# Optimization experiments

Measured on AMD Instinct MI355X. Metric: run time of the kernel, lower is better.

## Reference

```python
import jax, jax.numpy as jnp
import numpy as np

# Quantum circuit closed form: per wire i, state |0> -> RX(x_i) -> RY(theta_i),
# then <PauliZ_i> = cos(theta_i) * cos(x_i). No entangling gates, so wires are
# independent and the whole per-token loop collapses to one elementwise op.

B, S, E = 8, 4096, 512
NQ, FFN = 8, 2048

def setup_inputs() -> dict:
    key = jax.random.key(0)
    ks = jax.random.split(key, 6)
    return {
        "x": jax.random.normal(ks[0], (B, S, E), dtype=jnp.float32),
        "theta": jax.random.normal(ks[1], (NQ,), dtype=jnp.float32),
        "W1": jax.random.normal(ks[2], (FFN, NQ), dtype=jnp.float32) * (1.0 / np.sqrt(NQ)),
        "b1": jax.random.normal(ks[3], (FFN,), dtype=jnp.float32) * 0.01,
        "W2": jax.random.normal(ks[4], (E, FFN), dtype=jnp.float32) * (1.0 / np.sqrt(FFN)),
        "b2": jax.random.normal(ks[5], (E,), dtype=jnp.float32) * 0.01,
    }

def reference(x, theta, W1, b1, W2, b2):
    n_qubits = theta.shape[0]
    # token_slice = x[:, :, :n_qubits]; <Z> = cos(theta) * cos(x)
    q_out = jnp.cos(x[..., :n_qubits]) * jnp.cos(theta)        # [B, S, NQ]
    h = jax.nn.relu(jnp.einsum('bsq,fq->bsf', q_out, W1) + b1)  # [B, S, FFN]
    out = jnp.einsum('bsf,ef->bse', h, W2) + b2                 # [B, S, E]
    return out
```

## Files before the change

### kernel.cpp

```cpp
#include <hip/hip_runtime.h>
#include <math.h>

typedef __attribute__((ext_vector_type(8)))  short short8;
typedef __attribute__((ext_vector_type(4)))  short short4_t;
typedef __attribute__((ext_vector_type(16))) float float16_t;

__device__ __forceinline__ short f2bf(float f) {
    union { float f; unsigned u; } c; c.f = f;
    unsigned u = c.u + 0x7fffu + ((c.u >> 16) & 1u);
    return (short)(u >> 16);
}
__device__ __forceinline__ float16_t zero16() {
    float16_t z;
#pragma unroll
    for (int r = 0; r < 16; ++r) z[r] = 0.0f;
    return z;
}

__global__ __launch_bounds__(256) void prep_kernel(
    const float* __restrict__ x, const float* __restrict__ theta,
    const float* __restrict__ W1, const float* __restrict__ W2,
    short* __restrict__ W2P, short* __restrict__ Qz, short* __restrict__ W1z)
{
    int gid = blockIdx.x * 256 + threadIdx.x;
    if (gid < 131072) {
        int lane = gid & 63;
        int ks   = (gid >> 6) & 127;
        int nt   = gid >> 13;
        int n = nt * 32 + (lane & 31);
        int k = ks * 16 + (lane >> 5) * 8;
        const float4* p = (const float4*)(W2 + n * 2048 + k);
        float4 v0 = p[0], v1 = p[1];
        short8 o;
        o[0] = f2bf(v0.x); o[1] = f2bf(v0.y); o[2] = f2bf(v0.z); o[3] = f2bf(v0.w);
        o[4] = f2bf(v1.x); o[5] = f2bf(v1.y); o[6] = f2bf(v1.z); o[7] = f2bf(v1.w);
        *(short8*)(W2P + gid * 8) = o;
    } else if (gid < 131072 + 32768) {
        int t = gid - 131072;
        const float4* xp = (const float4*)(x + t * 512);
        float4 x0 = xp[0], x1 = xp[1];
        float xv[8] = {x0.x, x0.y, x0.z, x0.w, x1.x, x1.y, x1.z, x1.w};
        short8 q;
#pragma unroll
        for (int c = 0; c < 8; ++c)
            q[c] = f2bf(cosf(xv[c]) * cosf(theta[c]));
        *(short8*)(Qz + t * 8) = q;
    } else if (gid < 131072 + 32768 + 2048) {
        int f = gid - (131072 + 32768);
        const float4* wp = (const float4*)(W1 + f * 8);
        float4 w0 = wp[0], w1 = wp[1];
        short8 wv;
        wv[0] = f2bf(w0.x); wv[1] = f2bf(w0.y); wv[2] = f2bf(w0.z); wv[3] = f2bf(w0.w);
        wv[4] = f2bf(w1.x); wv[5] = f2bf(w1.y); wv[6] = f2bf(w1.z); wv[7] = f2bf(w1.w);
        short8 z = {0,0,0,0,0,0,0,0};
        *(short8*)(W1z + f * 16) = wv;
        *(short8*)(W1z + f * 16 + 8) = z;
    }
}

__global__ __launch_bounds__(256, 2) void ffn_kernel(
    const short* __restrict__ Qz, const short* __restrict__ W1z,
    const short* __restrict__ W2P, const float* __restrict__ b1,
    const float* __restrict__ b2, float* __restrict__ out)
{
    __shared__ short Hs[8 * 1024];

    const int tid  = threadIdx.x;
    const int lane = tid & 63;
    const int w    = tid >> 6;
    const int wx = w & 1, wy = w >> 1;
    const int l31 = lane & 31, lh = lane >> 5;
    const int bid = blockIdx.x;
    const int nt = bid & 3, mt = bid >> 2;
    const int m0 = mt * 128, n0 = nt * 128;
    const int s1_ft = w & 1, s1_mh = w >> 1;

    short8 qf[2];
#pragma unroll
    for (int i = 0; i < 2; ++i) {
        short8 v = {0,0,0,0,0,0,0,0};
        if (lh == 0)
            v = *(const short8*)(Qz + (m0 + s1_mh * 64 + i * 32 + l31) * 8);
        qf[i] = v;
    }

    float16_t acc[2][2];
#pragma unroll
    for (int i = 0; i < 2; ++i)
#pragma unroll
        for (int j = 0; j < 2; ++j) acc[i][j] = zero16();

    for (int kt = 0; kt < 32; ++kt) {
        const int k0 = kt * 64;

        short8 a1 = *(const short8*)(W1z + (k0 + s1_ft * 32 + l31) * 16 + lh * 8);

        float4 bsv[4];
#pragma unroll
        for (int g = 0; g < 4; ++g)
            bsv[g] = *(const float4*)(b1 + k0 + s1_ft * 32 + 4 * lh + 8 * g);

        short8 bf[4][2];
#pragma unroll
        for (int ks = 0; ks < 4; ++ks)
#pragma unroll
            for (int j = 0; j < 2; ++j)
                bf[ks][j] = *(const short8*)(W2P +
                    (((nt * 4 + wx * 2 + j) * 128 + (kt * 4 + ks)) * 64 + lane) * 8);

        __syncthreads();

#pragma unroll
        for (int i = 0; i < 2; ++i) {
            float16_t d1 = __builtin_amdgcn_mfma_f32_32x32x16_bf16(
                a1, qf[i], zero16(), 0, 0, 0);
            const int m = s1_mh * 64 + i * 32 + l31;
#pragma unroll
            for (int g = 0; g < 4; ++g) {
                float bb[4] = {bsv[g].x, bsv[g].y, bsv[g].z, bsv[g].w};
                short4_t p;
#pragma unroll
                for (int r = 0; r < 4; ++r) {
                    float h = d1[g * 4 + r] + bb[r];
                    h = fmaxf(h, 0.0f);
                    p[r] = f2bf(h);
                }
                *(short4_t*)(Hs + (s1_ft * 4 + g) * 1024 + m * 8 + 4 * lh) = p;
            }
        }
        __syncthreads();

#pragma unroll
        for (int ks = 0; ks < 4; ++ks) {
            short8 af[2];
#pragma unroll
            for (int i = 0; i < 2; ++i)
                af[i] = *(const short8*)(Hs + (ks * 2 + lh) * 1024 +
                                         (wy * 64 + i * 32 + l31) * 8);
#pragma unroll
            for (int i = 0; i < 2; ++i)
#pragma unroll
                for (int j = 0; j < 2; ++j)
                    acc[i][j] = __builtin_amdgcn_mfma_f32_32x32x16_bf16(
                        af[i], bf[ks][j], acc[i][j], 0, 0, 0);
        }
    }

#pragma unroll
    for (int j = 0; j < 2; ++j) {
        const int n = n0 + wx * 64 + j * 32 + l31;
        const float b2v = b2[n];
#pragma unroll
        for (int i = 0; i < 2; ++i) {
            const int mbase = m0 + wy * 64 + i * 32 + 4 * lh;
#pragma unroll
            for (int r = 0; r < 16; ++r) {
                const int row = mbase + (r & 3) + 8 * (r >> 2);
                out[row * 512 + n] = acc[i][j][r] + b2v;
            }
        }
    }
}

extern "C" void kernel_launch(void* const* d_in, const int* in_sizes, int n_in,
                              void* d_out, int out_size, void* d_ws, size_t ws_size,
                              hipStream_t stream)
{
    const float* x     = (const float*)d_in[0];
    const float* theta = (const float*)d_in[1];
    const float* W1    = (const float*)d_in[2];
    const float* b1    = (const float*)d_in[3];
    const float* W2    = (const float*)d_in[4];
    const float* b2    = (const float*)d_in[5];
    float* out = (float*)d_out;

    short* W2P = (short*)d_ws;
    short* Qz  = (short*)((char*)d_ws + 2097152);
    short* W1z = (short*)((char*)d_ws + 2621440);

    prep_kernel<<<648, 256, 0, stream>>>(x, theta, W1, W2, W2P, Qz, W1z);
    ffn_kernel<<<1024, 256, 0, stream>>>(Qz, W1z, W2P, b1, b2, out);
}
```

Baseline: 202.3 us.

## Widen output tile to 128x256 and double-buffer hidden tile in LDS

Each block now computes a 128x256 output tile (grid 512 instead of 1024), so the first GEMM (recomputing the hidden activations) is repeated half as often across N tiles. The shared hidden buffer is double-buffered, so the next k-step's stage-1 MFMA and ReLU overlap with the current stage-2 MFMAs, leaving one barrier per iteration instead of two. W2 fragments are loaded per ks inside the loop rather than prefetched for the whole k-tile. The accumulator doubles to 8 tiles per wave, which raises register pressure and may reduce occupancy under launch bounds of 2.

After: 186.2 us. -8.0%, faster.

```diff
diff --git a/kernel.cpp b/kernel.cpp
--- a/kernel.cpp
+++ b/kernel.cpp
@@ -58,97 +58,103 @@
     }
 }
 
+__device__ __forceinline__ void stage1_tile(
+    const short* __restrict__ W1z, const float* __restrict__ b1,
+    short* __restrict__ dst, const short8* qf,
+    int k0, int wx, int wy, int lh, int l31)
+{
+    short8 a1 = *(const short8*)(W1z + (k0 + wx * 32 + l31) * 16 + lh * 8);
+    float4 bsv[4];
+#pragma unroll
+    for (int g = 0; g < 4; ++g)
+        bsv[g] = *(const float4*)(b1 + k0 + wx * 32 + 4 * lh + 8 * g);
+#pragma unroll
+    for (int i = 0; i < 2; ++i) {
+        float16_t d1 = __builtin_amdgcn_mfma_f32_32x32x16_bf16(
+            a1, qf[i], zero16(), 0, 0, 0);
+        const int m = wy * 64 + i * 32 + l31;
+#pragma unroll
+        for (int g = 0; g < 4; ++g) {
+            float bb[4] = {bsv[g].x, bsv[g].y, bsv[g].z, bsv[g].w};
+            short4_t p;
+#pragma unroll
+            for (int r = 0; r < 4; ++r) {
+                float h = d1[g * 4 + r] + bb[r];
+                h = fmaxf(h, 0.0f);
+                p[r] = f2bf(h);
+            }
+            *(short4_t*)(dst + (wx * 4 + g) * 1024 + m * 8 + 4 * lh) = p;
+        }
+    }
+}
+
 __global__ __launch_bounds__(256, 2) void ffn_kernel(
     const short* __restrict__ Qz, const short* __restrict__ W1z,
     const short* __restrict__ W2P, const float* __restrict__ b1,
     const float* __restrict__ b2, float* __restrict__ out)
 {
-    __shared__ short Hs[8 * 1024];
+    __shared__ short Hs[2 * 8192];
 
     const int tid  = threadIdx.x;
     const int lane = tid & 63;
     const int w    = tid >> 6;
-    const int wx = w & 1, wy = w >> 1;
+    const int wy = w & 1, wx = w >> 1;
     const int l31 = lane & 31, lh = lane >> 5;
     const int bid = blockIdx.x;
-    const int nt = bid & 3, mt = bid >> 2;
-    const int m0 = mt * 128, n0 = nt * 128;
-    const int s1_ft = w & 1, s1_mh = w >> 1;
+    const int nt = bid & 1, mt = bid >> 1;
+    const int m0 = mt * 128, n0 = nt * 256;
 
     short8 qf[2];
 #pragma unroll
     for (int i = 0; i < 2; ++i) {
         short8 v = {0,0,0,0,0,0,0,0};
         if (lh == 0)
-            v = *(const short8*)(Qz + (m0 + s1_mh * 64 + i * 32 + l31) * 8);
+            v = *(const short8*)(Qz + (m0 + wy * 64 + i * 32 + l31) * 8);
         qf[i] = v;
     }
 
-    float16_t acc[2][2];
+    float16_t acc[2][4];
 #pragma unroll
     for (int i = 0; i < 2; ++i)
 #pragma unroll
-        for (int j = 0; j < 2; ++j) acc[i][j] = zero16();
+        for (int j = 0; j < 4; ++j) acc[i][j] = zero16();
+
+    stage1_tile(W1z, b1, Hs, qf, 0, wx, wy, lh, l31);
+    __syncthreads();
 
     for (int kt = 0; kt < 32; ++kt) {
-        const int k0 = kt * 64;
+        const int p = kt & 1;
+        const short* rd = Hs + p * 8192;
 
-        short8 a1 = *(const short8*)(W1z + (k0 + s1_ft * 32 + l31) * 16 + lh * 8);
-
-        float4 bsv[4];
-#pragma unroll
-        for (int g = 0; g < 4; ++g)
-            bsv[g] = *(const float4*)(b1 + k0 + s1_ft * 32 + 4 * lh + 8 * g);
-
-        short8 bf[4][2];
-#pragma unroll
-        for (int ks = 0; ks < 4; ++ks)
-#pragma unroll
-            for (int j = 0; j < 2; ++j)
-                bf[ks][j] = *(const short8*)(W2P +
-                    (((nt * 4 + wx * 2 + j) * 128 + (kt * 4 + ks)) * 64 + lane) * 8);
-
-        __syncthreads();
-
-#pragma unroll
-        for (int i = 0; i < 2; ++i) {
-            float16_t d1 = __builtin_amdgcn_mfma_f32_32x32x16_bf16(
-                a1, qf[i], zero16(), 0, 0, 0);
-            const int m = s1_mh * 64 + i * 32 + l31;
-#pragma unroll
-            for (int g = 0; g < 4; ++g) {
-                float bb[4] = {bsv[g].x, bsv[g].y, bsv[g].z, bsv[g].w};
-                short4_t p;
-#pragma unroll
-                for (int r = 0; r < 4; ++r) {
-                    float h = d1[g * 4 + r] + bb[r];
-                    h = fmaxf(h, 0.0f);
-                    p[r] = f2bf(h);
-                }
-                *(short4_t*)(Hs + (s1_ft * 4 + g) * 1024 + m * 8 + 4 * lh) = p;
-            }
-        }
-        __syncthreads();
+        if (kt < 31)
+            stage1_tile(W1z, b1, Hs + (p ^ 1) * 8192, qf,
+                        (kt + 1) * 64, wx, wy, lh, l31);
 
 #pragma unroll
         for (int ks = 0; ks < 4; ++ks) {
+            short8 bf[4];
+#pragma unroll
+            for (int j = 0; j < 4; ++j)
+                bf[j] = *(const short8*)(W2P +
+                    (((nt * 8 + wx * 4 + j) * 128 + (kt * 4 + ks)) * 64 + lane) * 8);
             short8 af[2];
 #pragma unroll
             for (int i = 0; i < 2; ++i)
-                af[i] = *(const short8*)(Hs + (ks * 2 + lh) * 1024 +
+                af[i] = *(const short8*)(rd + (ks * 2 + lh) * 1024 +
                                          (wy * 64 + i * 32 + l31) * 8);
 #pragma unroll
             for (int i = 0; i < 2; ++i)
 #pragma unroll
-                for (int j = 0; j < 2; ++j)
+                for (int j = 0; j < 4; ++j)
                     acc[i][j] = __builtin_amdgcn_mfma_f32_32x32x16_bf16(
-                        af[i], bf[ks][j], acc[i][j], 0, 0, 0);
+                        af[i], bf[j], acc[i][j], 0, 0, 0);
         }
+        __syncthreads();
     }
 
 #pragma unroll
-    for (int j = 0; j < 2; ++j) {
-        const int n = n0 + wx * 64 + j * 32 + l31;
+    for (int j = 0; j < 4; ++j) {
+        const int n = n0 + wx * 128 + j * 32 + l31;
         const float b2v = b2[n];
 #pragma unroll
         for (int i = 0; i < 2; ++i) {
@@ -179,5 +185,5 @@
     short* W1z = (short*)((char*)d_ws + 2621440);
 
     prep_kernel<<<648, 256, 0, stream>>>(x, theta, W1, W2, W2P, Qz, W1z);
-    ffn_kernel<<<1024, 256, 0, stream>>>(Qz, W1z, W2P, b1, b2, out);
+    ffn_kernel<<<512, 256, 0, stream>>>(Qz, W1z, W2P, b1, b2, out);
 }
```
